# Kernel optimization log

Measured on AMD Instinct MI355X. Metric: run time of the kernel, lower is better.

## Reference

```python
import jax, jax.numpy as jnp
import numpy as np

N = 100000      # total nodes across all graphs
E = 1600000     # total directed edges (pred -> node)
F = 128         # feat_size
H = 128         # hidden_size
M = 128         # message_size
G = 8           # number of graphs in batch
NP = N // G     # nodes per graph (num_nodes entries, all equal)
CRITIC_W = 0.5  # critic_agg_weight


def _lin_init(key, fan_in, fan_out):
    s = 1.0 / np.sqrt(fan_in)
    return jax.random.uniform(key, (fan_in, fan_out), jnp.float32, -s, s)


def setup_inputs() -> dict:
    key = jax.random.key(0)
    ks = jax.random.split(key, 20)
    inputs = jax.random.normal(ks[0], (N, F), jnp.float32)
    edge_src = jax.random.randint(ks[1], (E,), 0, N)
    edge_dst = jax.random.randint(ks[2], (E,), 0, N)
    actions = jax.random.randint(ks[3], (G,), 0, NP)
    return {
        'inputs': inputs,
        'W_in': _lin_init(ks[4], F, H), 'b_in': jnp.zeros((H,), jnp.float32),
        'W_msg': _lin_init(ks[5], H, M), 'b_msg': jnp.zeros((M,), jnp.float32),
        'W_upd': _lin_init(ks[6], M + H, H), 'b_upd': jnp.zeros((H,), jnp.float32),
        'W_a1': _lin_init(ks[7], H, 16), 'b_a1': jnp.zeros((16,), jnp.float32),
        'W_a2': _lin_init(ks[8], 16, 1), 'b_a2': jnp.zeros((1,), jnp.float32),
        'W_c1': _lin_init(ks[9], H, 16), 'b_c1': jnp.zeros((16,), jnp.float32),
        'W_c2': _lin_init(ks[10], 16, 1), 'b_c2': jnp.zeros((1,), jnp.float32),
        'edge_src': edge_src, 'edge_dst': edge_dst, 'actions': actions,
    }


def reference(inputs, W_in, b_in, W_msg, b_msg, W_upd, b_upd,
              W_a1, b_a1, W_a2, b_a2, W_c1, b_c1, W_c2, b_c2,
              edge_src, edge_dst, actions):
    # InputModel: Linear + ReLU  (send_input=True)
    node_states = jax.nn.relu(inputs @ W_in + b_in)          # [N, H]
    # MessageModel: Linear + ReLU
    messages = jax.nn.relu(node_states @ W_msg + b_msg)      # [N, M]
    # _aggregate_all: per-node sum over predecessor messages (segment-sum over edges)
    agg = jax.ops.segment_sum(messages[edge_src], edge_dst, num_segments=N)  # [N, M]
    # UpdateModel: Linear(M+H, H) + ReLU (no goal)
    updates = jax.nn.relu(jnp.concatenate([agg, node_states], axis=1) @ W_upd + b_upd)  # [N, H]
    # ActorModel: per-node logit
    logits_all = (jax.nn.relu(updates @ W_a1 + b_a1) @ W_a2 + b_a2).reshape(G, NP)
    # CriticModel: per-node score, per-graph weighted max/mean pooling
    crit_all = (jax.nn.relu(updates @ W_c1 + b_c1) @ W_c2 + b_c2).reshape(G, NP)
    v = (crit_all.max(axis=1) * CRITIC_W + crit_all.mean(axis=1) * (1.0 - CRITIC_W))[:, None]  # [G,1]
    # Categorical(logits) per graph: log_prob of given action + entropy
    logp = jax.nn.log_softmax(logits_all, axis=1)            # [G, NP]
    log_prob = jnp.take_along_axis(logp, actions[:, None], axis=1)  # [G,1]
    ent = -jnp.sum(jnp.exp(logp) * logp, axis=1, keepdims=True)     # [G,1]
    return updates, actions, log_prob, ent, v
```

## Files before the change

kernel.cpp:

```cpp
#include <hip/hip_runtime.h>
#include <math.h>

typedef unsigned short u16;
typedef unsigned int   u32;
typedef unsigned char  u8;
typedef __attribute__((ext_vector_type(8))) short short8v;
typedef __attribute__((ext_vector_type(4))) float f32x4;
typedef __attribute__((ext_vector_type(2))) float f32x2;

__device__ __forceinline__ u16 f2bf(float x) {
    u32 u = __float_as_uint(x);
    u += 0x7FFFu + ((u >> 16) & 1u);
    return (u16)(u >> 16);
}

#if __has_builtin(__builtin_amdgcn_cvt_pk_fp8_f32) && __has_builtin(__builtin_amdgcn_cvt_pk_f32_fp8)
#define HW_FP8 1
#endif

__device__ __forceinline__ u8 f2fp8(float v) {
#ifdef HW_FP8
    return (u8)(__builtin_amdgcn_cvt_pk_fp8_f32(v, v, 0, false) & 0xFF);
#else
    if (v < 0.015625f) return (u8)__float2int_rn(v * 512.0f);
    u32 b = __float_as_uint(fminf(v, 448.0f));
    b += 0x7FFFF + ((b >> 20) & 1);
    return (u8)((((b >> 23) - 120) << 3) | ((b >> 20) & 7));
#endif
}

__device__ __forceinline__ void fp8x4_acc(u32 w, float* acc) {
#ifdef HW_FP8
    const f32x2 lo = __builtin_amdgcn_cvt_pk_f32_fp8(w, false);
    const f32x2 hi = __builtin_amdgcn_cvt_pk_f32_fp8(w, true);
    acc[0] += lo[0]; acc[1] += lo[1]; acc[2] += hi[0]; acc[3] += hi[1];
#else
#pragma unroll
    for (int i = 0; i < 4; ++i) {
        const u32 b = (w >> (8 * i)) & 0xFF;
        const u32 e = (b >> 3) & 15, m = b & 7;
        acc[i] += e ? __uint_as_float(((e + 120) << 23) | (m << 20))
                    : (float)m * 0x1p-9f;
    }
#endif
}

#define NPB        256
#define NPB_SHIFT  8
#define EBUF_CAP   4608
#define MAX_BUK    512
#define BCS        16
#define BIN_CHUNK  4096

__global__ __launch_bounds__(1024) void convbin_kernel(
    const float* __restrict__ W_in, const float* __restrict__ W_msg,
    const float* __restrict__ W_upd,
    const float* __restrict__ Wa1, const float* __restrict__ Wc1,
    u16* __restrict__ Wt_in, u16* __restrict__ Wt_msg,
    u16* __restrict__ Wt_upd, u16* __restrict__ Wh,
    const int* __restrict__ src, const int* __restrict__ dst,
    int* __restrict__ bcursor, int* __restrict__ ebuf,
    int E, int nbuk, int convBlocks)
{
    __shared__ int lcount[MAX_BUK];
    __shared__ int lbase[MAX_BUK];
    const int tid = threadIdx.x;

    if ((int)blockIdx.x < convBlocks) {
        const int idx = blockIdx.x * 1024 + tid;
        if (idx < 16384) {
            const int c = idx >> 7, k = idx & 127;
            Wt_in[c * 128 + k] = f2bf(W_in[k * 128 + c]);
        } else if (idx < 32768) {
            const int i = idx - 16384;
            const int c = i >> 7, k = i & 127;
            Wt_msg[c * 128 + k] = f2bf(W_msg[k * 128 + c]);
        } else if (idx < 65536) {
            const int i = idx - 32768;
            const int c = i >> 8, k = i & 255;
            Wt_upd[c * 256 + k] = f2bf(W_upd[k * 128 + c]);
        } else if (idx < 69632) {
            const int i = idx - 65536;
            const int col = i >> 7, k = i & 127;
            const float v = (col < 16) ? Wa1[k * 16 + col] : Wc1[k * 16 + (col - 16)];
            Wh[col * 128 + k] = f2bf(v);
        }
        return;
    }

    const int e0 = (blockIdx.x - convBlocks) * BIN_CHUNK;
    const int e1 = min(e0 + BIN_CHUNK, E);
    for (int b = tid; b < nbuk; b += 1024) lcount[b] = 0;
    __syncthreads();

    int pay[4];
    u32 brk[4];
#pragma unroll
    for (int k = 0; k < 4; ++k) {
        const int i = e0 + tid + k * 1024;
        int payv = 0; u32 brkv = 0xFFFFFFFFu;
        if (i < e1) {
            const int d = dst[i];
            const int b = d >> NPB_SHIFT;
            const int r = atomicAdd(&lcount[b], 1);
            payv = (src[i] << NPB_SHIFT) | (d & (NPB - 1));
            brkv = ((u32)b << 16) | (u32)r;
        }
        pay[k] = payv; brk[k] = brkv;
    }
    __syncthreads();

    for (int b = tid; b < nbuk; b += 1024) {
        const int c = lcount[b];
        lbase[b] = c ? atomicAdd(&bcursor[b * BCS], c) : 0;
    }
    __syncthreads();

#pragma unroll
    for (int k = 0; k < 4; ++k) {
        if (brk[k] != 0xFFFFFFFFu) {
            const int b = (int)(brk[k] >> 16);
            const int p = lbase[b] + (int)(brk[k] & 0xFFFFu);
            ebuf[b * EBUF_CAP + min(p, EBUF_CAP - 1)] = pay[k];
        }
    }
}

__global__ __launch_bounds__(256) void csr_gemm1_kernel(
    const int* __restrict__ ebuf, const int* __restrict__ bcursor,
    int* __restrict__ offs, int* __restrict__ csr, int N, int E, int nbuk,
    const float* __restrict__ X, const u16* __restrict__ Wt_in,
    const float* __restrict__ b_in, u16* __restrict__ ns, int rows)
{
    __shared__ u16 smem[128 * 136];
    const int tid = threadIdx.x;

    if ((int)blockIdx.x < nbuk) {
        int* ibuf = (int*)smem;
        int* red  = ibuf;
        int* ndeg = ibuf + 4;
        int* nofs = ibuf + 260;
        int* ws   = ibuf + 516;
        int* wp   = ibuf + 520;
        const int b = blockIdx.x;

        int part = 0;
        for (int i = tid; i < b; i += 256) part += bcursor[i * BCS];
#pragma unroll
        for (int off = 32; off >= 1; off >>= 1) part += __shfl_xor(part, off);
        if ((tid & 63) == 0) red[tid >> 6] = part;
        __syncthreads();
        const int base = red[0] + red[1] + red[2] + red[3];

        const int cnt = min(bcursor[b * BCS], EBUF_CAP);
        const int* eb = ebuf + b * EBUF_CAP;

        ndeg[tid] = 0;
        __syncthreads();
        for (int j = tid; j < cnt; j += 256)
            atomicAdd(&ndeg[eb[j] & (NPB - 1)], 1);
        __syncthreads();

        const int lane = tid & 63, wid = tid >> 6;
        const int v = ndeg[tid];
        int x = v;
#pragma unroll
        for (int off = 1; off < 64; off <<= 1) {
            const int y = __shfl_up(x, off);
            if (lane >= off) x += y;
        }
        if (lane == 63) ws[wid] = x;
        __syncthreads();
        if (tid == 0) { int s = 0; for (int w = 0; w < 4; ++w) { wp[w] = s; s += ws[w]; } }
        __syncthreads();
        const int excl = x - v + wp[wid];
        nofs[tid] = excl;
        const int node = (b << NPB_SHIFT) + tid;
        if (node < N) offs[node] = base + excl;
        if (b == 0 && tid == 0) offs[N] = E;
        ndeg[tid] = 0;
        __syncthreads();

        for (int j = tid; j < cnt; j += 256) {
            const int e = eb[j];
            const int d = e & (NPB - 1);
            const int p = atomicAdd(&ndeg[d], 1);
            csr[base + nofs[d] + p] = e >> NPB_SHIFT;
        }
        return;
    }

    u16 (*WtL)[136] = (u16(*)[136])smem;
    for (int i = tid; i < 2048; i += 256)
        *(uint4*)&WtL[i >> 4][(i & 15) * 8] = ((const uint4*)Wt_in)[i];

    const int lane = tid & 63, wave = tid >> 6;
    const int lrow = lane & 15, lk = lane >> 4;
    const int r0 = (blockIdx.x - nbuk) * 64 + wave * 16;
    const int arow = r0 + lrow;
    const bool rowok = arow < rows;

    short8v a[4];
#pragma unroll
    for (int ks = 0; ks < 4; ++ks) {
        const int k = ks * 32 + lk * 8;
        short8v av = {};
        if (rowok) {
            const float* pf = X + (size_t)arow * 128 + k;
            const float4 x0 = *(const float4*)pf;
            const float4 x1 = *(const float4*)(pf + 4);
            u16 t[8] = {f2bf(x0.x), f2bf(x0.y), f2bf(x0.z), f2bf(x0.w),
                        f2bf(x1.x), f2bf(x1.y), f2bf(x1.z), f2bf(x1.w)};
            av = *(short8v*)t;
        }
        a[ks] = av;
    }
    __syncthreads();

    f32x4 acc[8];
#pragma unroll
    for (int n = 0; n < 8; ++n) acc[n] = (f32x4){0.f, 0.f, 0.f, 0.f};
#pragma unroll
    for (int ks = 0; ks < 4; ++ks) {
#pragma unroll
        for (int n = 0; n < 8; ++n) {
            const short8v b = *(const short8v*)&WtL[n * 16 + lrow][ks * 32 + lk * 8];
            acc[n] = __builtin_amdgcn_mfma_f32_16x16x32_bf16(a[ks], b, acc[n], 0, 0, 0);
        }
    }
#pragma unroll
    for (int reg = 0; reg < 4; ++reg) {
        const int row = r0 + lk * 4 + reg;
        if (row >= rows) continue;
#pragma unroll
        for (int n = 0; n < 8; ++n) {
            const float v = fmaxf(acc[n][reg] + b_in[n * 16 + lrow], 0.f);
            ns[(size_t)row * 128 + n * 16 + lrow] = f2bf(v);
        }
    }
}

__global__ __launch_bounds__(512) void gemm2_kernel(
    const u16* __restrict__ ns, const u16* __restrict__ Wt_msg,
    const float* __restrict__ b_msg, u8* __restrict__ msg8, int rows)
{
    __shared__ u16 smem[128 * 136];
    u16 (*WtL)[136] = (u16(*)[136])smem;
    const int tid = threadIdx.x;
    for (int i = tid; i < 2048; i += 512)
        *(uint4*)&WtL[i >> 4][(i & 15) * 8] = ((const uint4*)Wt_msg)[i];

    const int lane = tid & 63, wave = tid >> 6;
    const int lrow = lane & 15, lk = lane >> 4;
    const int r0 = blockIdx.x * 128 + wave * 16;
    const int arow = r0 + lrow;
    const bool rowok = arow < rows;

    short8v a[4];
#pragma unroll
    for (int ks = 0; ks < 4; ++ks) {
        short8v av = {};
        if (rowok) av = *(const short8v*)(ns + (size_t)arow * 128 + ks * 32 + lk * 8);
        a[ks] = av;
    }
    __syncthreads();

    f32x4 acc[8];
#pragma unroll
    for (int n = 0; n < 8; ++n) acc[n] = (f32x4){0.f, 0.f, 0.f, 0.f};
#pragma unroll
    for (int ks = 0; ks < 4; ++ks) {
#pragma unroll
        for (int n = 0; n < 8; ++n) {
            const short8v b = *(const short8v*)&WtL[n * 16 + lrow][ks * 32 + lk * 8];
            acc[n] = __builtin_amdgcn_mfma_f32_16x16x32_bf16(a[ks], b, acc[n], 0, 0, 0);
        }
    }
#pragma unroll
    for (int reg = 0; reg < 4; ++reg) {
        const int row = r0 + lk * 4 + reg;
        if (row >= rows) continue;
#pragma unroll
        for (int n = 0; n < 8; ++n) {
            const float v = fmaxf(acc[n][reg] + b_msg[n * 16 + lrow], 0.f);
            msg8[(size_t)row * 128 + n * 16 + lrow] = f2fp8(v);
        }
    }
}

__device__ __forceinline__ void acc16(float* acc, const uint4 u) {
    fp8x4_acc(u.x, acc);
    fp8x4_acc(u.y, acc + 4);
    fp8x4_acc(u.z, acc + 8);
    fp8x4_acc(u.w, acc + 12);
}

__global__ __launch_bounds__(256) void gather_fp8_kernel(
    const int* __restrict__ offs, const int* __restrict__ csr,
    const u8* __restrict__ msg8, u16* __restrict__ agg, int N)
{
    const int node = blockIdx.x * 32 + (threadIdx.x >> 3);
    if (node >= N) return;
    const int c16 = threadIdx.x & 7;
    int j = offs[node];
    const int j1 = offs[node + 1];
    const uint4* mv = (const uint4*)msg8;
    float acc[16];
#pragma unroll
    for (int q = 0; q < 16; ++q) acc[q] = 0.f;
    for (; j + 3 < j1; j += 4) {
        const int s0 = csr[j], s1 = csr[j + 1], s2 = csr[j + 2], s3 = csr[j + 3];
        const uint4 u0 = mv[(size_t)s0 * 8 + c16];
        const uint4 u1 = mv[(size_t)s1 * 8 + c16];
        const uint4 u2 = mv[(size_t)s2 * 8 + c16];
        const uint4 u3 = mv[(size_t)s3 * 8 + c16];
        acc16(acc, u0); acc16(acc, u1); acc16(acc, u2); acc16(acc, u3);
    }
    for (; j < j1; ++j)
        acc16(acc, mv[(size_t)csr[j] * 8 + c16]);

    u16 r[16];
#pragma unroll
    for (int q = 0; q < 16; ++q) r[q] = f2bf(acc[q]);
    uint4* ap = (uint4*)(agg + (size_t)node * 128 + c16 * 16);
    ap[0] = *(uint4*)r;
    ap[1] = *(uint4*)(r + 8);
}

__global__ __launch_bounds__(512) void gemm3_head_kernel(
    const u16* __restrict__ agg, const u16* __restrict__ ns,
    const u16* __restrict__ Wt_upd, const float* __restrict__ b_upd,
    float* __restrict__ Cf,
    const u16* __restrict__ Wh,
    const float* __restrict__ ba1, const float* __restrict__ Wa2, const float* __restrict__ ba2,
    const float* __restrict__ bc1, const float* __restrict__ Wc2, const float* __restrict__ bc2,
    float* __restrict__ logits, float* __restrict__ crit, int rows)
{
    __shared__ u16 smem[128 * 136];
    u16 (*WtL)[136] = (u16(*)[136])smem;

    const int tid = threadIdx.x;
    const uint4* W4 = (const uint4*)Wt_upd;

    for (int i = tid; i < 2048; i += 512)
        *(uint4*)&WtL[i >> 4][(i & 15) * 8] = W4[(i >> 4) * 32 + (i & 15)];

    const int lane = tid & 63, wave = tid >> 6;
    const int lrow = lane & 15, lk = lane >> 4;
    const int r0 = blockIdx.x * 128 + wave * 16;
    const int arow = r0 + lrow;
    const bool rowok = arow < rows;

    short8v a[4], a2[4];
#pragma unroll
    for (int ks = 0; ks < 4; ++ks) {
        short8v av = {}, av2 = {};
        if (rowok) {
            av  = *(const short8v*)(agg + (size_t)arow * 128 + ks * 32 + lk * 8);
            av2 = *(const short8v*)(ns  + (size_t)arow * 128 + ks * 32 + lk * 8);
        }
        a[ks] = av; a2[ks] = av2;
    }
    __syncthreads();

    f32x4 acc[8];
#pragma unroll
    for (int n = 0; n < 8; ++n) acc[n] = (f32x4){0.f, 0.f, 0.f, 0.f};
#pragma unroll
    for (int ks = 0; ks < 4; ++ks) {
#pragma unroll
        for (int n = 0; n < 8; ++n) {
            const short8v b = *(const short8v*)&WtL[n * 16 + lrow][ks * 32 + lk * 8];
            acc[n] = __builtin_amdgcn_mfma_f32_16x16x32_bf16(a[ks], b, acc[n], 0, 0, 0);
        }
    }

    __syncthreads();
    for (int i = tid; i < 2048; i += 512)
        *(uint4*)&WtL[i >> 4][(i & 15) * 8] = W4[(i >> 4) * 32 + 16 + (i & 15)];
    __syncthreads();

#pragma unroll
    for (int ks = 0; ks < 4; ++ks) {
#pragma unroll
        for (int n = 0; n < 8; ++n) {
            const short8v b = *(const short8v*)&WtL[n * 16 + lrow][ks * 32 + lk * 8];
            acc[n] = __builtin_amdgcn_mfma_f32_16x16x32_bf16(a2[ks], b, acc[n], 0, 0, 0);
        }
    }

    u16 uv[4][8];
#pragma unroll
    for (int reg = 0; reg < 4; ++reg) {
        const int row = r0 + lk * 4 + reg;
#pragma unroll
        for (int n = 0; n < 8; ++n) {
            const float v = fmaxf(acc[n][reg] + b_upd[n * 16 + lrow], 0.f);
            uv[reg][n] = f2bf(v);
            if (row < rows) Cf[(size_t)row * 128 + n * 16 + lrow] = v;
        }
    }
    __syncthreads();

    u16 (*uT)[16][136] = (u16(*)[16][136])smem;
#pragma unroll
    for (int reg = 0; reg < 4; ++reg) {
        const int lr = lk * 4 + reg;
#pragma unroll
        for (int n = 0; n < 8; ++n)
            uT[wave][lr][n * 16 + lrow] = uv[reg][n];
    }
    __syncthreads();

    short8v ah[4], b0[4], b1[4];
#pragma unroll
    for (int ks = 0; ks < 4; ++ks) {
        const int k = ks * 32 + lk * 8;
        ah[ks] = *(const short8v*)&uT[wave][lrow][k];
        b0[ks] = *(const short8v*)(Wh + (size_t)lrow * 128 + k);
        b1[ks] = *(const short8v*)(Wh + (size_t)(16 + lrow) * 128 + k);
    }
    f32x4 acc0 = (f32x4){0.f, 0.f, 0.f, 0.f};
    f32x4 acc1 = (f32x4){0.f, 0.f, 0.f, 0.f};
#pragma unroll
    for (int ks = 0; ks < 4; ++ks) {
        acc0 = __builtin_amdgcn_mfma_f32_16x16x32_bf16(ah[ks], b0[ks], acc0, 0, 0, 0);
        acc1 = __builtin_amdgcn_mfma_f32_16x16x32_bf16(ah[ks], b1[ks], acc1, 0, 0, 0);
    }
    const float wa = Wa2[lrow], wc = Wc2[lrow];
    const float ha = ba1[lrow], hc = bc1[lrow];
    const float b2a = ba2[0],   b2c = bc2[0];
#pragma unroll
    for (int reg = 0; reg < 4; ++reg) {
        float pa = fmaxf(acc0[reg] + ha, 0.f) * wa;
        float pc = fmaxf(acc1[reg] + hc, 0.f) * wc;
#pragma unroll
        for (int off = 8; off >= 1; off >>= 1) {
            pa += __shfl_xor(pa, off);
            pc += __shfl_xor(pc, off);
        }
        const int row = r0 + lk * 4 + reg;
        if (lrow == 0 && row < rows) {
            logits[row] = pa + b2a;
            crit[row]   = pc + b2c;
        }
    }
}

__device__ __forceinline__ float blockRedMax(float v, float* red) {
#pragma unroll
    for (int o = 32; o >= 1; o >>= 1) v = fmaxf(v, __shfl_xor(v, o));
    const int w = threadIdx.x >> 6;
    __syncthreads();
    if ((threadIdx.x & 63) == 0) red[w] = v;
    __syncthreads();
    if (threadIdx.x < 16) {
        float x = red[threadIdx.x];
#pragma unroll
        for (int o = 8; o >= 1; o >>= 1) x = fmaxf(x, __shfl_xor(x, o));
        if (threadIdx.x == 0) red[0] = x;
    }
    __syncthreads();
    const float r = red[0];
    __syncthreads();
    return r;
}

__device__ __forceinline__ float blockRedSum(float v, float* red) {
#pragma unroll
    for (int o = 32; o >= 1; o >>= 1) v += __shfl_xor(v, o);
    const int w = threadIdx.x >> 6;
    __syncthreads();
    if ((threadIdx.x & 63) == 0) red[w] = v;
    __syncthreads();
    if (threadIdx.x < 16) {
        float x = red[threadIdx.x];
#pragma unroll
        for (int o = 8; o >= 1; o >>= 1) x += __shfl_xor(x, o);
        if (threadIdx.x == 0) red[0] = x;
    }
    __syncthreads();
    const float r = red[0];
    __syncthreads();
    return r;
}

__global__ __launch_bounds__(1024) void finalize_kernel(
    const float* __restrict__ logits, const float* __restrict__ crit,
    const int* __restrict__ actions, float* __restrict__ out, int NP, int G)
{
    __shared__ float slog[12512];
    __shared__ float red[16];
    const int g = blockIdx.x;
    const int tid = threadIdx.x;
    const float* lg = logits + (long long)g * NP;
    const float* cg = crit   + (long long)g * NP;

    float lmax = -3.402823466e38f, cmax = -3.402823466e38f, csum = 0.f;
    for (int i = tid; i < NP; i += 1024) {
        const float l = lg[i], c = cg[i];
        slog[i] = l;
        lmax = fmaxf(lmax, l);
        cmax = fmaxf(cmax, c);
        csum += c;
    }
    __syncthreads();
    lmax = blockRedMax(lmax, red);
    cmax = blockRedMax(cmax, red);
    csum = blockRedSum(csum, red);

    float zsum = 0.f, ssum = 0.f;
    for (int i = tid; i < NP; i += 1024) {
        const float s = slog[i];
        const float e = expf(s - lmax);
        zsum += e;
        ssum += s * e;
    }
    zsum = blockRedSum(zsum, red);
    ssum = blockRedSum(ssum, red);

    if (tid == 0) {
        const int a = actions[g];
        const float sa   = slog[a];
        const float logZ = logf(zsum) + lmax;
        const float lp   = sa - logZ;
        const float H    = logZ - ssum / zsum;
        const float v    = cmax * 0.5f + (csum / (float)NP) * 0.5f;
        out[g]         = (float)a;
        out[G + g]     = lp;
        out[2 * G + g] = H;
        out[3 * G + g] = v;
    }
}

extern "C" void kernel_launch(void* const* d_in, const int* in_sizes, int n_in,
                              void* d_out, int out_size, void* d_ws, size_t ws_size,
                              hipStream_t stream)
{
    const float* inputs = (const float*)d_in[0];
    const float* W_in   = (const float*)d_in[1];
    const float* b_in   = (const float*)d_in[2];
    const float* W_msg  = (const float*)d_in[3];
    const float* b_msg  = (const float*)d_in[4];
    const float* W_upd  = (const float*)d_in[5];
    const float* b_upd  = (const float*)d_in[6];
    const float* W_a1   = (const float*)d_in[7];
    const float* b_a1   = (const float*)d_in[8];
    const float* W_a2   = (const float*)d_in[9];
    const float* b_a2   = (const float*)d_in[10];
    const float* W_c1   = (const float*)d_in[11];
    const float* b_c1   = (const float*)d_in[12];
    const float* W_c2   = (const float*)d_in[13];
    const float* b_c2   = (const float*)d_in[14];
    const int* edge_src = (const int*)d_in[15];
    const int* edge_dst = (const int*)d_in[16];
    const int* actions  = (const int*)d_in[17];

    const int N  = in_sizes[0] / 128;
    const int E  = in_sizes[15];
    const int G  = in_sizes[17];
    const int NP = N / G;
    const int nbuk = (N + NPB - 1) >> NPB_SHIFT;

    float* out = (float*)d_out;

    u16* ns_bf  = (u16*)d_ws;
    u16* agg_bf = ns_bf + (size_t)N * 128;
    u8*  msg8   = (u8*)(agg_bf + (size_t)N * 128);
    u16* Wt_in  = (u16*)(msg8 + (size_t)N * 128);
    u16* Wt_msg = Wt_in  + 128 * 128;
    u16* Wt_upd = Wt_msg + 128 * 128;
    u16* Wh     = Wt_upd + 128 * 256;
    float* logits = (float*)(Wh + 32 * 128);
    float* crit   = logits + N;
    int*   offs    = (int*)(crit + N);
    int*   csr     = offs + (N + 1);
    int*   bcursor = csr + E;
    int*   ebuf    = bcursor + MAX_BUK * BCS;

    const int binGrid    = (E + BIN_CHUNK - 1) / BIN_CHUNK;
    const int convBlocks = 69632 / 1024;
    const int gemmGrid   = (N + 63) / 64;
    const int gemmGrid2  = (N + 127) / 128;

    hipMemsetAsync(bcursor, 0, (size_t)MAX_BUK * BCS * sizeof(int), stream);
    convbin_kernel<<<convBlocks + binGrid, 1024, 0, stream>>>(
        W_in, W_msg, W_upd, W_a1, W_c1, Wt_in, Wt_msg, Wt_upd, Wh,
        edge_src, edge_dst, bcursor, ebuf, E, nbuk, convBlocks);
    csr_gemm1_kernel<<<nbuk + gemmGrid, 256, 0, stream>>>(
        ebuf, bcursor, offs, csr, N, E, nbuk,
        inputs, Wt_in, b_in, ns_bf, N);
    gemm2_kernel<<<gemmGrid2, 512, 0, stream>>>(ns_bf, Wt_msg, b_msg, msg8, N);
    gather_fp8_kernel<<<(N + 31) / 32, 256, 0, stream>>>(offs, csr, msg8, agg_bf, N);
    gemm3_head_kernel<<<gemmGrid2, 512, 0, stream>>>(
        agg_bf, ns_bf, Wt_upd, b_upd, out, Wh,
        b_a1, W_a2, b_a2, b_c1, W_c2, b_c2, logits, crit, N);
    finalize_kernel<<<G, 1024, 0, stream>>>(logits, crit, actions, out + (size_t)N * 128, NP, G);
}
```

Measured before the change: 155.1 us.

## Regroup kernels: fold memset into weight conversion, pair binning with GEMM1

Splits weight conversion into its own small kernel that also zeroes the bucket cursors, which removes the separate hipMemsetAsync. Edge binning now shares a launch with the first GEMM, and CSR construction shares a launch with the message GEMM, so the irregular graph work overlaps the dense GEMM work in each launch. GEMM1 now runs with 1024-thread blocks covering 256 rows, and GEMM2 with 256-thread blocks covering 64 rows. The risk is heavier blocks and lower occupancy for the GEMM parts, and GEMM2 blocks sharing a launch with CSR buckets that may straggle.

```diff
diff --git a/kernel.cpp b/kernel.cpp
--- a/kernel.cpp
+++ b/kernel.cpp
@@ -52,151 +52,95 @@
 #define BCS        16
 #define BIN_CHUNK  4096
 
-__global__ __launch_bounds__(1024) void convbin_kernel(
+__global__ __launch_bounds__(256) void conv_kernel(
     const float* __restrict__ W_in, const float* __restrict__ W_msg,
     const float* __restrict__ W_upd,
     const float* __restrict__ Wa1, const float* __restrict__ Wc1,
     u16* __restrict__ Wt_in, u16* __restrict__ Wt_msg,
     u16* __restrict__ Wt_upd, u16* __restrict__ Wh,
+    int* __restrict__ bcursor)
+{
+    const int idx = blockIdx.x * 256 + threadIdx.x;
+    if (idx < 16384) {
+        const int c = idx >> 7, k = idx & 127;
+        Wt_in[c * 128 + k] = f2bf(W_in[k * 128 + c]);
+    } else if (idx < 32768) {
+        const int i = idx - 16384;
+        const int c = i >> 7, k = i & 127;
+        Wt_msg[c * 128 + k] = f2bf(W_msg[k * 128 + c]);
+    } else if (idx < 65536) {
+        const int i = idx - 32768;
+        const int c = i >> 8, k = i & 255;
+        Wt_upd[c * 256 + k] = f2bf(W_upd[k * 128 + c]);
+    } else if (idx < 69632) {
+        const int i = idx - 65536;
+        const int col = i >> 7, k = i & 127;
+        const float v = (col < 16) ? Wa1[k * 16 + col] : Wc1[k * 16 + (col - 16)];
+        Wh[col * 128 + k] = f2bf(v);
+    } else if (idx < 69632 + MAX_BUK * BCS) {
+        bcursor[idx - 69632] = 0;
+    }
+}
+
+__global__ __launch_bounds__(1024) void bin_gemm1_kernel(
     const int* __restrict__ src, const int* __restrict__ dst,
     int* __restrict__ bcursor, int* __restrict__ ebuf,
-    int E, int nbuk, int convBlocks)
-{
-    __shared__ int lcount[MAX_BUK];
-    __shared__ int lbase[MAX_BUK];
-    const int tid = threadIdx.x;
-
-    if ((int)blockIdx.x < convBlocks) {
-        const int idx = blockIdx.x * 1024 + tid;
-        if (idx < 16384) {
-            const int c = idx >> 7, k = idx & 127;
-            Wt_in[c * 128 + k] = f2bf(W_in[k * 128 + c]);
-        } else if (idx < 32768) {
-            const int i = idx - 16384;
-            const int c = i >> 7, k = i & 127;
-            Wt_msg[c * 128 + k] = f2bf(W_msg[k * 128 + c]);
-        } else if (idx < 65536) {
-            const int i = idx - 32768;
-            const int c = i >> 8, k = i & 255;
-            Wt_upd[c * 256 + k] = f2bf(W_upd[k * 128 + c]);
-        } else if (idx < 69632) {
-            const int i = idx - 65536;
-            const int col = i >> 7, k = i & 127;
-            const float v = (col < 16) ? Wa1[k * 16 + col] : Wc1[k * 16 + (col - 16)];
-            Wh[col * 128 + k] = f2bf(v);
-        }
-        return;
-    }
-
-    const int e0 = (blockIdx.x - convBlocks) * BIN_CHUNK;
-    const int e1 = min(e0 + BIN_CHUNK, E);
-    for (int b = tid; b < nbuk; b += 1024) lcount[b] = 0;
-    __syncthreads();
-
-    int pay[4];
-    u32 brk[4];
-#pragma unroll
-    for (int k = 0; k < 4; ++k) {
-        const int i = e0 + tid + k * 1024;
-        int payv = 0; u32 brkv = 0xFFFFFFFFu;
-        if (i < e1) {
-            const int d = dst[i];
-            const int b = d >> NPB_SHIFT;
-            const int r = atomicAdd(&lcount[b], 1);
-            payv = (src[i] << NPB_SHIFT) | (d & (NPB - 1));
-            brkv = ((u32)b << 16) | (u32)r;
-        }
-        pay[k] = payv; brk[k] = brkv;
-    }
-    __syncthreads();
-
-    for (int b = tid; b < nbuk; b += 1024) {
-        const int c = lcount[b];
-        lbase[b] = c ? atomicAdd(&bcursor[b * BCS], c) : 0;
-    }
-    __syncthreads();
-
-#pragma unroll
-    for (int k = 0; k < 4; ++k) {
-        if (brk[k] != 0xFFFFFFFFu) {
-            const int b = (int)(brk[k] >> 16);
-            const int p = lbase[b] + (int)(brk[k] & 0xFFFFu);
-            ebuf[b * EBUF_CAP + min(p, EBUF_CAP - 1)] = pay[k];
-        }
-    }
-}
-
-__global__ __launch_bounds__(256) void csr_gemm1_kernel(
-    const int* __restrict__ ebuf, const int* __restrict__ bcursor,
-    int* __restrict__ offs, int* __restrict__ csr, int N, int E, int nbuk,
+    int E, int nbuk, int binGrid,
     const float* __restrict__ X, const u16* __restrict__ Wt_in,
     const float* __restrict__ b_in, u16* __restrict__ ns, int rows)
 {
     __shared__ u16 smem[128 * 136];
     const int tid = threadIdx.x;
 
-    if ((int)blockIdx.x < nbuk) {
-        int* ibuf = (int*)smem;
-        int* red  = ibuf;
-        int* ndeg = ibuf + 4;
-        int* nofs = ibuf + 260;
-        int* ws   = ibuf + 516;
-        int* wp   = ibuf + 520;
-        const int b = blockIdx.x;
-
-        int part = 0;
-        for (int i = tid; i < b; i += 256) part += bcursor[i * BCS];
-#pragma unroll
-        for (int off = 32; off >= 1; off >>= 1) part += __shfl_xor(part, off);
-        if ((tid & 63) == 0) red[tid >> 6] = part;
-        __syncthreads();
-        const int base = red[0] + red[1] + red[2] + red[3];
-
-        const int cnt = min(bcursor[b * BCS], EBUF_CAP);
-        const int* eb = ebuf + b * EBUF_CAP;
-
-        ndeg[tid] = 0;
-        __syncthreads();
-        for (int j = tid; j < cnt; j += 256)
-            atomicAdd(&ndeg[eb[j] & (NPB - 1)], 1);
-        __syncthreads();
-
-        const int lane = tid & 63, wid = tid >> 6;
-        const int v = ndeg[tid];
-        int x = v;
-#pragma unroll
-        for (int off = 1; off < 64; off <<= 1) {
-            const int y = __shfl_up(x, off);
-            if (lane >= off) x += y;
-        }
-        if (lane == 63) ws[wid] = x;
-        __syncthreads();
-        if (tid == 0) { int s = 0; for (int w = 0; w < 4; ++w) { wp[w] = s; s += ws[w]; } }
-        __syncthreads();
-        const int excl = x - v + wp[wid];
-        nofs[tid] = excl;
-        const int node = (b << NPB_SHIFT) + tid;
-        if (node < N) offs[node] = base + excl;
-        if (b == 0 && tid == 0) offs[N] = E;
-        ndeg[tid] = 0;
-        __syncthreads();
-
-        for (int j = tid; j < cnt; j += 256) {
-            const int e = eb[j];
-            const int d = e & (NPB - 1);
-            const int p = atomicAdd(&ndeg[d], 1);
-            csr[base + nofs[d] + p] = e >> NPB_SHIFT;
+    if ((int)blockIdx.x < binGrid) {
+        int* lcount = (int*)smem;
+        int* lbase  = lcount + MAX_BUK;
+        const int e0 = blockIdx.x * BIN_CHUNK;
+        const int e1 = min(e0 + BIN_CHUNK, E);
+        for (int b = tid; b < nbuk; b += 1024) lcount[b] = 0;
+        __syncthreads();
+
+        int pay[4];
+        u32 brk[4];
+#pragma unroll
+        for (int k = 0; k < 4; ++k) {
+            const int i = e0 + tid + k * 1024;
+            int payv = 0; u32 brkv = 0xFFFFFFFFu;
+            if (i < e1) {
+                const int d = dst[i];
+                const int b = d >> NPB_SHIFT;
+                const int r = atomicAdd(&lcount[b], 1);
+                payv = (src[i] << NPB_SHIFT) | (d & (NPB - 1));
+                brkv = ((u32)b << 16) | (u32)r;
+            }
+            pay[k] = payv; brk[k] = brkv;
+        }
+        __syncthreads();
+
+        for (int b = tid; b < nbuk; b += 1024) {
+            const int c = lcount[b];
+            lbase[b] = c ? atomicAdd(&bcursor[b * BCS], c) : 0;
+        }
+        __syncthreads();
+
+#pragma unroll
+        for (int k = 0; k < 4; ++k) {
+            if (brk[k] != 0xFFFFFFFFu) {
+                const int b = (int)(brk[k] >> 16);
+                const int p = lbase[b] + (int)(brk[k] & 0xFFFFu);
+                ebuf[b * EBUF_CAP + min(p, EBUF_CAP - 1)] = pay[k];
+            }
         }
         return;
     }
 
     u16 (*WtL)[136] = (u16(*)[136])smem;
-    for (int i = tid; i < 2048; i += 256)
+    for (int i = tid; i < 2048; i += 1024)
         *(uint4*)&WtL[i >> 4][(i & 15) * 8] = ((const uint4*)Wt_in)[i];
 
     const int lane = tid & 63, wave = tid >> 6;
     const int lrow = lane & 15, lk = lane >> 4;
-    const int r0 = (blockIdx.x - nbuk) * 64 + wave * 16;
+    const int r0 = (blockIdx.x - binGrid) * 256 + wave * 16;
     const int arow = r0 + lrow;
     const bool rowok = arow < rows;
 
@@ -240,19 +184,77 @@
     }
 }
 
-__global__ __launch_bounds__(512) void gemm2_kernel(
+__global__ __launch_bounds__(256) void csr_gemm2_kernel(
+    const int* __restrict__ ebuf, const int* __restrict__ bcursor,
+    int* __restrict__ offs, int* __restrict__ csr, int N, int E, int nbuk,
     const u16* __restrict__ ns, const u16* __restrict__ Wt_msg,
     const float* __restrict__ b_msg, u8* __restrict__ msg8, int rows)
 {
     __shared__ u16 smem[128 * 136];
+    const int tid = threadIdx.x;
+
+    if ((int)blockIdx.x < nbuk) {
+        int* ibuf = (int*)smem;
+        int* red  = ibuf;
+        int* ndeg = ibuf + 4;
+        int* nofs = ibuf + 260;
+        int* ws   = ibuf + 516;
+        int* wp   = ibuf + 520;
+        const int b = blockIdx.x;
+
+        int part = 0;
+        for (int i = tid; i < b; i += 256) part += bcursor[i * BCS];
+#pragma unroll
+        for (int off = 32; off >= 1; off >>= 1) part += __shfl_xor(part, off);
+        if ((tid & 63) == 0) red[tid >> 6] = part;
+        __syncthreads();
+        const int base = red[0] + red[1] + red[2] + red[3];
+
+        const int cnt = min(bcursor[b * BCS], EBUF_CAP);
+        const int* eb = ebuf + b * EBUF_CAP;
+
+        ndeg[tid] = 0;
+        __syncthreads();
+        for (int j = tid; j < cnt; j += 256)
+            atomicAdd(&ndeg[eb[j] & (NPB - 1)], 1);
+        __syncthreads();
+
+        const int lane = tid & 63, wid = tid >> 6;
+        const int v = ndeg[tid];
+        int x = v;
+#pragma unroll
+        for (int off = 1; off < 64; off <<= 1) {
+            const int y = __shfl_up(x, off);
+            if (lane >= off) x += y;
+        }
+        if (lane == 63) ws[wid] = x;
+        __syncthreads();
+        if (tid == 0) { int s = 0; for (int w = 0; w < 4; ++w) { wp[w] = s; s += ws[w]; } }
+        __syncthreads();
+        const int excl = x - v + wp[wid];
+        nofs[tid] = excl;
+        const int node = (b << NPB_SHIFT) + tid;
+        if (node < N) offs[node] = base + excl;
+        if (b == 0 && tid == 0) offs[N] = E;
+        ndeg[tid] = 0;
+        __syncthreads();
+
+        for (int j = tid; j < cnt; j += 256) {
+            const int e = eb[j];
+            const int d = e & (NPB - 1);
+            const int p = atomicAdd(&ndeg[d], 1);
+            csr[base + nofs[d] + p] = e >> NPB_SHIFT;
+        }
+        return;
+    }
+
     u16 (*WtL)[136] = (u16(*)[136])smem;
-    const int tid = threadIdx.x;
-    for (int i = tid; i < 2048; i += 512)
+    for (int i = tid; i < 2048; i += 256)
         *(uint4*)&WtL[i >> 4][(i & 15) * 8] = ((const uint4*)Wt_msg)[i];
 
     const int lane = tid & 63, wave = tid >> 6;
     const int lrow = lane & 15, lk = lane >> 4;
-    const int r0 = blockIdx.x * 128 + wave * 16;
+    const int r0 = (blockIdx.x - nbuk) * 64 + wave * 16;
     const int arow = r0 + lrow;
     const bool rowok = arow < rows;
 
@@ -578,21 +580,22 @@
     int*   bcursor = csr + E;
     int*   ebuf    = bcursor + MAX_BUK * BCS;
 
-    const int binGrid    = (E + BIN_CHUNK - 1) / BIN_CHUNK;
-    const int convBlocks = 69632 / 1024;
-    const int gemmGrid   = (N + 63) / 64;
-    const int gemmGrid2  = (N + 127) / 128;
-
-    hipMemsetAsync(bcursor, 0, (size_t)MAX_BUK * BCS * sizeof(int), stream);
-    convbin_kernel<<<convBlocks + binGrid, 1024, 0, stream>>>(
-        W_in, W_msg, W_upd, W_a1, W_c1, Wt_in, Wt_msg, Wt_upd, Wh,
-        edge_src, edge_dst, bcursor, ebuf, E, nbuk, convBlocks);
-    csr_gemm1_kernel<<<nbuk + gemmGrid, 256, 0, stream>>>(
+    const int binGrid = (E + BIN_CHUNK - 1) / BIN_CHUNK;
+    const int convGrid = (69632 + MAX_BUK * BCS + 255) / 256;
+    const int g1Grid  = (N + 255) / 256;
+    const int g2Grid  = (N + 63) / 64;
+    const int g3Grid  = (N + 127) / 128;
+
+    conv_kernel<<<convGrid, 256, 0, stream>>>(
+        W_in, W_msg, W_upd, W_a1, W_c1, Wt_in, Wt_msg, Wt_upd, Wh, bcursor);
+    bin_gemm1_kernel<<<binGrid + g1Grid, 1024, 0, stream>>>(
+        edge_src, edge_dst, bcursor, ebuf, E, nbuk, binGrid,
+        inputs, Wt_in, b_in, ns_bf, N);
+    csr_gemm2_kernel<<<nbuk + g2Grid, 256, 0, stream>>>(
         ebuf, bcursor, offs, csr, N, E, nbuk,
-        inputs, Wt_in, b_in, ns_bf, N);
-    gemm2_kernel<<<gemmGrid2, 512, 0, stream>>>(ns_bf, Wt_msg, b_msg, msg8, N);
+        ns_bf, Wt_msg, b_msg, msg8, N);
     gather_fp8_kernel<<<(N + 31) / 32, 256, 0, stream>>>(offs, csr, msg8, agg_bf, N);
-    gemm3_head_kernel<<<gemmGrid2, 512, 0, stream>>>(
+    gemm3_head_kernel<<<g3Grid, 512, 0, stream>>>(
         agg_bf, ns_bf, Wt_upd, b_upd, out, Wh,
         b_a1, W_a2, b_a2, b_c1, W_c2, b_c2, logits, crit, N);
     finalize_kernel<<<G, 1024, 0, stream>>>(logits, crit, actions, out + (size_t)N * 128, NP, G);
```

Measured after the change: 148.0 us. 1.05x faster.
